# Optimization experiments

Hardware: AMD Instinct MI355X
Metric: run time of the kernel (lower is better)

Reference implementation:

```python
import jax, jax.numpy as jnp
import numpy as np

E, H, D = 512, 8, 64          # embed_dim, num_heads, head_dim
MAX_SUM = 128                  # max_summary (embedding table has MAX_SUM+1 rows, row 0 = padding)
SCALE = D ** -0.5


def _linear(x, w, b):
    y = jnp.einsum('...i,oi->...o', x, w)
    return y if b is None else y + b


def setup_inputs() -> dict:
    key = jax.random.key(0)
    ks = jax.random.split(key, 16)
    R, B, S = 2048, 2, 128

    def xav(k, shape, gain=1.0):
        fan_in, fan_out = shape[1], shape[0]
        a = gain * np.sqrt(6.0 / (fan_in + fan_out))
        return jax.random.uniform(k, shape, jnp.float32, -a, a)

    g = 1.0 / np.sqrt(2.0)
    embed_table = jax.random.normal(ks[0], (MAX_SUM + 1, E), jnp.float32) * 0.02
    embed_table = embed_table.at[0].set(0.0)  # padding_idx=0
    return {
        'reg_x': jax.random.normal(ks[1], (R, B, E), jnp.float32),
        'sum_token_ids': jax.random.randint(ks[2], (B, S), 0, MAX_SUM),
        'sum_len': S,
        'reg_len': R,
        'embed_table': embed_table,
        'wq1': xav(ks[3], (E, E), g), 'bq1': jnp.zeros((E,), jnp.float32),
        'wq2': xav(ks[4], (E, E), g), 'bq2': jnp.zeros((E,), jnp.float32),
        'wk': xav(ks[5], (E, E), g),  'bk': jnp.zeros((E,), jnp.float32),
        'wv': xav(ks[6], (E, E), g),  'bv': jnp.zeros((E,), jnp.float32),
        'wo': xav(ks[7], (E, E)),     'bo': jnp.zeros((E,), jnp.float32),
        'sum_gate_w': xav(ks[8], (E, E)),
        'reg_gate_w': xav(ks[9], (E, E)),
        'gate_bias': jax.random.normal(ks[10], (E,), jnp.float32),
    }


def reference(reg_x, sum_token_ids, sum_len, reg_len, embed_table,
              wq1, bq1, wq2, bq2, wk, bk, wv, bv, wo, bo,
              sum_gate_w, reg_gate_w, gate_bias):
    R, B, _ = reg_x.shape
    S = sum_token_ids.shape[1]

    # regular keys/values (shared across all stages)
    reg_k = _linear(reg_x, wk, bk).reshape(R, B, H, D)
    reg_v = _linear(reg_x, wv, bv).reshape(R, B, H, D)

    # ---- stage 1: summary queries (learned summary embeddings) attend to regular tokens
    sum_q = embed_table[sum_token_ids.T].reshape(S, B, H, D)  # [S,B,H,D]
    scores_sr = jnp.einsum('sbhd,rbhd->bhsr', sum_q * SCALE, reg_k)
    w_sr = jax.nn.softmax(scores_sr, axis=-1)
    sum_x2 = jnp.einsum('bhsr,rbhd->sbhd', w_sr, reg_v)       # summary K=V for stage 2

    # ---- stage 2: regular queries attend to summary tokens
    reg_q1 = _linear(reg_x, wq1, bq1).reshape(R, B, H, D)
    scores_rs = jnp.einsum('rbhd,sbhd->bhrs', reg_q1 * SCALE, sum_x2)
    w_rs = jax.nn.softmax(scores_rs, axis=-1)
    sum_output = jnp.einsum('bhrs,sbhd->rbhd', w_rs, sum_x2).reshape(R, B, E)

    # ---- stage 3: regular self-attention
    reg_q2 = _linear(reg_x, wq2, bq2).reshape(R, B, H, D)
    scores_rr = jnp.einsum('qbhd,kbhd->bhqk', reg_q2 * SCALE, reg_k)
    w_rr = jax.nn.softmax(scores_rr, axis=-1)
    reg_output = jnp.einsum('bhqk,kbhd->qbhd', w_rr, reg_v).reshape(R, B, E)

    # ---- gated fusion of summary path and regular path
    gate = jax.nn.sigmoid(_linear(sum_output, sum_gate_w, None)
                          + _linear(reg_output, reg_gate_w, None) + gate_bias)
    attn_output = gate * sum_output + (1.0 - gate) * reg_output
    return _linear(attn_output, wo, bo)
```

## Files before the change

kernel.cpp:

```cpp
#include <hip/hip_runtime.h>
#include <cstdint>
#include <cstddef>

constexpr int R_ = 2048;
constexpr int B_ = 2;
constexpr int S_ = 128;
constexpr int E_ = 512;
constexpr int H_ = 8;
constexpr int D_ = 64;
constexpr int N_ = R_ * B_;
constexpr float SCALE_ = 0.125f;
constexpr float LOG2E_ = 1.44269504088896340736f;
constexpr float SLOG2E_ = SCALE_ * LOG2E_;

typedef short bf8_t __attribute__((ext_vector_type(8)));
typedef float f32x4 __attribute__((ext_vector_type(4)));
typedef float f32x16 __attribute__((ext_vector_type(16)));
typedef unsigned u32x4 __attribute__((ext_vector_type(4)));

#define MFMA16(a, b, c) __builtin_amdgcn_mfma_f32_16x16x32_bf16((a), (b), (c), 0, 0, 0)
#define MFMA32(a, b, c) __builtin_amdgcn_mfma_f32_32x32x16_bf16((a), (b), (c), 0, 0, 0)

__device__ __forceinline__ unsigned short f2bf(float f) {
  unsigned u = __builtin_bit_cast(unsigned, f);
  unsigned r = u + 0x7FFFu + ((u >> 16) & 1u);
  return (unsigned short)(r >> 16);
}
__device__ __forceinline__ float bf2f(unsigned short h) {
  unsigned u = ((unsigned)h) << 16;
  return __builtin_bit_cast(float, u);
}
__device__ __forceinline__ int kvperm(int kv) {
  return (kv & ~15) | (kv & 3) | ((kv & 4) << 1) | ((kv & 8) >> 1);
}

struct WSplitJob { const float* src; unsigned short* dst; };
struct WSplit7 { WSplitJob j[7]; };

__global__ __launch_bounds__(256)
void fused_split_kernel(const float* __restrict__ reg_x, unsigned short* __restrict__ Apair,
                        WSplit7 P, const float* __restrict__ table,
                        const int* __restrict__ ids,
                        unsigned short* __restrict__ sqhi, unsigned short* __restrict__ sqlo)
{
  const int bx = blockIdx.x;
  const int tid = threadIdx.x;
  if (bx < 8192) {
    const int idx = bx * 256 + tid;
    const int r = idx >> 9, c = idx & 511;
    const float v = reg_x[idx];
    const unsigned short hi = f2bf(v);
    unsigned short* d = Apair + ((size_t)r << 10) + c;
    d[0] = hi; d[512] = f2bf(v - bf2f(hi));
  } else if (bx < 15360) {
    const int bj = bx - 8192;
    const WSplitJob jb = P.j[bj >> 10];
    const int idx = (bj & 1023) * 256 + tid;
    const int r = idx >> 9, c = idx & 511;
    const float v = jb.src[idx];
    const unsigned short hi = f2bf(v);
    const unsigned short lo = f2bf(v - bf2f(hi));
    unsigned short* d = jb.dst + (size_t)r * 1536 + c;
    d[0] = hi; d[512] = hi; d[1024] = lo;
  } else {
    const int idx = (bx - 15360) * 256 + tid;
    const int d = idx & 63;
    const int s = (idx >> 6) & 127;
    const int h = (idx >> 13) & 7;
    const int b = idx >> 16;
    const float v = table[(size_t)ids[b * S_ + s] * E_ + h * 64 + d] * SLOG2E_;
    const unsigned short hi = f2bf(v);
    sqhi[idx] = hi;
    sqlo[idx] = f2bf(v - bf2f(hi));
  }
}

struct GemmOut {
  const unsigned short* W;
  const float* bias;
  float scale;
  float* Cf;
  unsigned short* hi;
  unsigned short* lo;
  int mode;
};
struct GemmOuts4 { GemmOut o[4]; };

__global__ __launch_bounds__(256, 4)
void gemm_split_kernel(const unsigned short* __restrict__ A, GemmOuts4 P)
{
  const GemmOut g = P.o[blockIdx.z];
  __shared__ unsigned short As[128][48];
  __shared__ unsigned short Ws[64][48];

  const int tid = threadIdx.x;
  const int w = tid >> 6;
  const int l = tid & 63;
  const int lr = l & 15;
  const int lg = l >> 4;
  const int n0 = blockIdx.x * 128;
  const int o0 = blockIdx.y * 64;

  f32x4 acc[2][4];
#pragma unroll
  for (int m = 0; m < 2; ++m)
#pragma unroll
    for (int n = 0; n < 4; ++n) acc[m][n] = (f32x4){0.f, 0.f, 0.f, 0.f};

  const int ar = tid >> 1;
  const int ac = (tid & 1) * 16;
  const int wr = tid >> 2;
  const int wc = (tid & 3) * 8;

  bf8_t ra0 = *(const bf8_t*)(A + (size_t)(n0 + ar) * 1024 + ac);
  bf8_t ra1 = *(const bf8_t*)(A + (size_t)(n0 + ar) * 1024 + ac + 8);
  bf8_t rw0 = *(const bf8_t*)(g.W + (size_t)(o0 + wr) * 1536 + wc);

  for (int k0 = 0; k0 < 1536; k0 += 32) {
    __syncthreads();
    *(bf8_t*)&As[ar][ac] = ra0;
    *(bf8_t*)&As[ar][ac + 8] = ra1;
    *(bf8_t*)&Ws[wr][wc] = rw0;
    __syncthreads();
    if (k0 + 32 < 1536) {
      const int ak = (k0 + 32) & 1023;
      ra0 = *(const bf8_t*)(A + (size_t)(n0 + ar) * 1024 + ak + ac);
      ra1 = *(const bf8_t*)(A + (size_t)(n0 + ar) * 1024 + ak + ac + 8);
      rw0 = *(const bf8_t*)(g.W + (size_t)(o0 + wr) * 1536 + k0 + 32 + wc);
    }

    bf8_t bvs[4];
#pragma unroll
    for (int n = 0; n < 4; ++n)
      bvs[n] = *(const bf8_t*)&Ws[n * 16 + lr][lg * 8];
#pragma unroll
    for (int m = 0; m < 2; ++m) {
      bf8_t av = *(const bf8_t*)&As[w * 32 + m * 16 + lr][lg * 8];
#pragma unroll
      for (int n = 0; n < 4; ++n)
        acc[m][n] = MFMA16(av, bvs[n], acc[m][n]);
    }
  }

#pragma unroll
  for (int m = 0; m < 2; ++m)
#pragma unroll
    for (int n = 0; n < 4; ++n)
#pragma unroll
      for (int r = 0; r < 4; ++r) {
        const int row = n0 + w * 32 + m * 16 + lg * 4 + r;
        const int col = o0 + n * 16 + lr;
        float v = acc[m][n][r];
        if (g.bias) v += g.bias[col];
        v *= g.scale;
        if (g.mode == 0) {
          g.Cf[((size_t)row << 9) + col] = v;
        } else {
          const int bb = row & 1, rr = row >> 1;
          const int hh = col >> 6, dd = col & 63;
          size_t id;
          if (g.mode == 1) id = (((size_t)(bb * H_ + hh) * R_) + rr) * 64 + dd;
          else             id = (((size_t)(bb * H_ + hh) * 64) + dd) * R_ + kvperm(rr);
          const unsigned short hv = f2bf(v);
          g.hi[id] = hv;
          g.lo[id] = f2bf(v - bf2f(hv));
        }
      }
}

__global__ __launch_bounds__(256, 4)
void gate_blend_gemm_kernel(const unsigned short* __restrict__ A1,
                            const unsigned short* __restrict__ A2,
                            const unsigned short* __restrict__ W1,
                            const unsigned short* __restrict__ W2,
                            const float* __restrict__ gb,
                            unsigned short* __restrict__ attnP)
{
  __shared__ unsigned short As[128][48];
  __shared__ unsigned short Ws[64][48];

  const int tid = threadIdx.x;
  const int w = tid >> 6;
  const int l = tid & 63;
  const int lr = l & 15;
  const int lg = l >> 4;
  const int n0 = blockIdx.x * 128;
  const int o0 = blockIdx.y * 64;

  f32x4 acc[2][4];
#pragma unroll
  for (int m = 0; m < 2; ++m)
#pragma unroll
    for (int n = 0; n < 4; ++n) acc[m][n] = (f32x4){0.f, 0.f, 0.f, 0.f};

  const int ar = tid >> 1;
  const int ac = (tid & 1) * 16;
  const int wr = tid >> 2;
  const int wc = (tid & 3) * 8;

  auto aP = [&](int kk) {
    const unsigned short* Ax = (kk < 48) ? A1 : A2;
    const int k0 = ((kk < 48) ? kk : kk - 48) * 32;
    return Ax + (size_t)(n0 + ar) * 1024 + (k0 & 1023) + ac;
  };
  auto wP = [&](int kk) {
    const unsigned short* Wx = (kk < 48) ? W1 : W2;
    const int k0 = ((kk < 48) ? kk : kk - 48) * 32;
    return Wx + (size_t)(o0 + wr) * 1536 + k0 + wc;
  };

  bf8_t ra0 = *(const bf8_t*)aP(0);
  bf8_t ra1 = *(const bf8_t*)(aP(0) + 8);
  bf8_t rw0 = *(const bf8_t*)wP(0);

  for (int kk = 0; kk < 96; ++kk) {
    __syncthreads();
    *(bf8_t*)&As[ar][ac] = ra0;
    *(bf8_t*)&As[ar][ac + 8] = ra1;
    *(bf8_t*)&Ws[wr][wc] = rw0;
    __syncthreads();
    if (kk + 1 < 96) {
      ra0 = *(const bf8_t*)aP(kk + 1);
      ra1 = *(const bf8_t*)(aP(kk + 1) + 8);
      rw0 = *(const bf8_t*)wP(kk + 1);
    }

    bf8_t bvs[4];
#pragma unroll
    for (int n = 0; n < 4; ++n)
      bvs[n] = *(const bf8_t*)&Ws[n * 16 + lr][lg * 8];
#pragma unroll
    for (int m = 0; m < 2; ++m) {
      bf8_t av = *(const bf8_t*)&As[w * 32 + m * 16 + lr][lg * 8];
#pragma unroll
      for (int n = 0; n < 4; ++n)
        acc[m][n] = MFMA16(av, bvs[n], acc[m][n]);
    }
  }

#pragma unroll
  for (int m = 0; m < 2; ++m)
#pragma unroll
    for (int n = 0; n < 4; ++n)
#pragma unroll
      for (int r = 0; r < 4; ++r) {
        const int row = n0 + w * 32 + m * 16 + lg * 4 + r;
        const int col = o0 + n * 16 + lr;
        const float t = acc[m][n][r] + gb[col];
        const float gt = 1.0f / (1.0f + __expf(-t));
        const size_t base = (size_t)row << 10;
        const float so = bf2f(A1[base + col]) + bf2f(A1[base + 512 + col]);
        const float ro = bf2f(A2[base + col]) + bf2f(A2[base + 512 + col]);
        const float a = gt * so + (1.0f - gt) * ro;
        const unsigned short hv = f2bf(a);
        attnP[base + col] = hv;
        attnP[base + 512 + col] = f2bf(a - bf2f(hv));
      }
}

__global__ __launch_bounds__(256, 2)
void flash_partial_kernel(const unsigned short* __restrict__ Qhi, const unsigned short* __restrict__ Qlo,
                          const unsigned short* __restrict__ Khi, const unsigned short* __restrict__ Klo,
                          const unsigned short* __restrict__ VtHi, const unsigned short* __restrict__ VtLo,
                          int q_len, int kv_len, int chunk, int zsplit, int out_mode,
                          float* __restrict__ accA, float* __restrict__ accB,
                          float* __restrict__ mlP, unsigned short* __restrict__ OutP)
{
  __shared__ unsigned short KsH[64][72];
  __shared__ unsigned short KsL[64][72];
  __shared__ unsigned short VsH[64][72];
  __shared__ unsigned short VsL[64][72];

  const int tid = threadIdx.x;
  const int w = tid >> 6;
  const int l = tid & 63;
  const int lq = l & 31;
  const int hi = l >> 5;
  const int bh = blockIdx.y;
  const int q0 = blockIdx.x * 128;
  const int c = blockIdx.z;
  const int kvbeg = c * chunk;
  const int kvend = kvbeg + chunk;
  const int qrow = q0 + w * 32 + lq;

  bf8_t qh[4], ql[4];
  {
    const size_t qbase = ((size_t)bh * q_len + qrow) * 64;
#pragma unroll
    for (int kd = 0; kd < 4; ++kd) {
      qh[kd] = *(const bf8_t*)(Qhi + qbase + kd * 16 + hi * 8);
      ql[kd] = *(const bf8_t*)(Qlo + qbase + kd * 16 + hi * 8);
    }
  }

  f32x16 acc0 = {0,0,0,0,0,0,0,0,0,0,0,0,0,0,0,0};
  f32x16 acc1 = {0,0,0,0,0,0,0,0,0,0,0,0,0,0,0,0};
  float mrow = -INFINITY;
  float lrow = 0.0f;

  const int sr = tid >> 2;
  const int sc = (tid & 3) * 16;

  bf8_t rkh[2], rkl[2], rvh[2], rvl[2];
  {
    const size_t kb = ((size_t)bh * kv_len + kvbeg + sr) * 64 + sc;
    rkh[0] = *(const bf8_t*)(Khi + kb);  rkh[1] = *(const bf8_t*)(Khi + kb + 8);
    rkl[0] = *(const bf8_t*)(Klo + kb);  rkl[1] = *(const bf8_t*)(Klo + kb + 8);
    const size_t vb = ((size_t)bh * 64 + sr) * kv_len + kvbeg + sc;
    rvh[0] = *(const bf8_t*)(VtHi + vb); rvh[1] = *(const bf8_t*)(VtHi + vb + 8);
    rvl[0] = *(const bf8_t*)(VtLo + vb); rvl[1] = *(const bf8_t*)(VtLo + vb + 8);
  }

  for (int kv0 = kvbeg; kv0 < kvend; kv0 += 64) {
    __syncthreads();
    *(bf8_t*)&KsH[sr][sc] = rkh[0];  *(bf8_t*)&KsH[sr][sc + 8] = rkh[1];
    *(bf8_t*)&KsL[sr][sc] = rkl[0];  *(bf8_t*)&KsL[sr][sc + 8] = rkl[1];
    *(bf8_t*)&VsH[sr][sc] = rvh[0];  *(bf8_t*)&VsH[sr][sc + 8] = rvh[1];
    *(bf8_t*)&VsL[sr][sc] = rvl[0];  *(bf8_t*)&VsL[sr][sc + 8] = rvl[1];
    __syncthreads();
    if (kv0 + 64 < kvend) {
      const size_t kb = ((size_t)bh * kv_len + kv0 + 64 + sr) * 64 + sc;
      rkh[0] = *(const bf8_t*)(Khi + kb);  rkh[1] = *(const bf8_t*)(Khi + kb + 8);
      rkl[0] = *(const bf8_t*)(Klo + kb);  rkl[1] = *(const bf8_t*)(Klo + kb + 8);
      const size_t vb = ((size_t)bh * 64 + sr) * kv_len + kv0 + 64 + sc;
      rvh[0] = *(const bf8_t*)(VtHi + vb); rvh[1] = *(const bf8_t*)(VtHi + vb + 8);
      rvl[0] = *(const bf8_t*)(VtLo + vb); rvl[1] = *(const bf8_t*)(VtLo + vb + 8);
    }

    f32x16 s0 = {0,0,0,0,0,0,0,0,0,0,0,0,0,0,0,0};
    f32x16 s1 = {0,0,0,0,0,0,0,0,0,0,0,0,0,0,0,0};
    __builtin_amdgcn_s_setprio(1);
#pragma unroll
    for (int kd = 0; kd < 4; ++kd) {
      const bf8_t kfh0 = *(const bf8_t*)&KsH[lq][kd * 16 + hi * 8];
      const bf8_t kfl0 = *(const bf8_t*)&KsL[lq][kd * 16 + hi * 8];
      s0 = MFMA32(kfh0, qh[kd], s0);
      s0 = MFMA32(kfh0, ql[kd], s0);
      s0 = MFMA32(kfl0, qh[kd], s0);
      const bf8_t kfh1 = *(const bf8_t*)&KsH[32 + lq][kd * 16 + hi * 8];
      const bf8_t kfl1 = *(const bf8_t*)&KsL[32 + lq][kd * 16 + hi * 8];
      s1 = MFMA32(kfh1, qh[kd], s1);
      s1 = MFMA32(kfh1, ql[kd], s1);
      s1 = MFMA32(kfl1, qh[kd], s1);
    }
    __builtin_amdgcn_s_setprio(0);

    float mx = fmaxf(s0[0], s1[0]);
#pragma unroll
    for (int r = 1; r < 16; ++r) mx = fmaxf(mx, fmaxf(s0[r], s1[r]));
    mx = fmaxf(mx, __shfl_xor(mx, 32));
    if (mx > mrow + 8.0f) {
      const float f = exp2f(mrow - mx);
      mrow = mx;
      lrow *= f;
#pragma unroll
      for (int r = 0; r < 16; ++r) { acc0[r] *= f; acc1[r] *= f; }
    }
    float ts = 0.f;
#pragma unroll
    for (int r = 0; r < 16; ++r) { s0[r] = exp2f(s0[r] - mrow); ts += s0[r]; }
#pragma unroll
    for (int r = 0; r < 16; ++r) { s1[r] = exp2f(s1[r] - mrow); ts += s1[r]; }
    ts += __shfl_xor(ts, 32);
    lrow += ts;

    bf8_t pah[4], pal[4];
#pragma unroll
    for (int n = 0; n < 2; ++n)
#pragma unroll
      for (int ks = 0; ks < 2; ++ks) {
        u32x4 hp, lp;
#pragma unroll
        for (int p2 = 0; p2 < 4; ++p2) {
          const float a = n ? s1[ks * 8 + p2 * 2]     : s0[ks * 8 + p2 * 2];
          const float b = n ? s1[ks * 8 + p2 * 2 + 1] : s0[ks * 8 + p2 * 2 + 1];
          const unsigned ua = __builtin_bit_cast(unsigned, a);
          const unsigned ub = __builtin_bit_cast(unsigned, b);
          hp[p2] = (ua >> 16) | (ub & 0xFFFF0000u);
          const float la = a - __builtin_bit_cast(float, ua & 0xFFFF0000u);
          const float lb = b - __builtin_bit_cast(float, ub & 0xFFFF0000u);
          lp[p2] = (__builtin_bit_cast(unsigned, la) >> 16) |
                   (__builtin_bit_cast(unsigned, lb) & 0xFFFF0000u);
        }
        pah[n * 2 + ks] = __builtin_bit_cast(bf8_t, hp);
        pal[n * 2 + ks] = __builtin_bit_cast(bf8_t, lp);
      }

    __builtin_amdgcn_s_setprio(1);
#pragma unroll
    for (int n = 0; n < 2; ++n)
#pragma unroll
      for (int ks = 0; ks < 2; ++ks) {
        const int vcol = n * 32 + ks * 16 + hi * 8;
        const bf8_t ph = pah[n * 2 + ks];
        const bf8_t pl = pal[n * 2 + ks];
        {
          const bf8_t vfh = *(const bf8_t*)&VsH[lq][vcol];
          const bf8_t vfl = *(const bf8_t*)&VsL[lq][vcol];
          acc0 = MFMA32(vfh, ph, acc0);
          acc0 = MFMA32(vfh, pl, acc0);
          acc0 = MFMA32(vfl, ph, acc0);
        }
        {
          const bf8_t vfh = *(const bf8_t*)&VsH[32 + lq][vcol];
          const bf8_t vfl = *(const bf8_t*)&VsL[32 + lq][vcol];
          acc1 = MFMA32(vfh, ph, acc1);
          acc1 = MFMA32(vfh, pl, acc1);
          acc1 = MFMA32(vfl, ph, acc1);
        }
      }
    __builtin_amdgcn_s_setprio(0);
  }

  if (out_mode == 0) {
    const size_t cstride = (size_t)16 * q_len * 64;
    float* accbase = (c < zsplit) ? accA + (size_t)c * cstride
                                  : accB + (size_t)(c - zsplit) * cstride;
    float* rowp = accbase + ((size_t)bh * q_len + qrow) * 64;
#pragma unroll
    for (int rg = 0; rg < 4; ++rg) {
      *(float4*)(rowp + rg * 8 + hi * 4) =
          make_float4(acc0[rg * 4 + 0], acc0[rg * 4 + 1], acc0[rg * 4 + 2], acc0[rg * 4 + 3]);
      *(float4*)(rowp + 32 + rg * 8 + hi * 4) =
          make_float4(acc1[rg * 4 + 0], acc1[rg * 4 + 1], acc1[rg * 4 + 2], acc1[rg * 4 + 3]);
    }
    if (l < 32) {
      const int q = q0 + w * 32 + l;
      *(float2*)&mlP[((size_t)(c * 16 + bh) * q_len + q) * 2] = make_float2(mrow, lrow);
    }
  } else {
    const float inv = 1.0f / lrow;
    const int b = bh >> 3, h = bh & 7;
    const size_t base = ((size_t)qrow * B_ + b) << 10;
#pragma unroll
    for (int hd = 0; hd < 2; ++hd)
#pragma unroll
      for (int rg = 0; rg < 4; ++rg) {
        const int col = h * 64 + hd * 32 + rg * 8 + hi * 4;
        ushort4 hv4, lv4;
#pragma unroll
        for (int i = 0; i < 4; ++i) {
          const float v = (hd ? acc1[rg * 4 + i] : acc0[rg * 4 + i]) * inv;
          const unsigned short hv = f2bf(v);
          ((unsigned short*)&hv4)[i] = hv;
          ((unsigned short*)&lv4)[i] = f2bf(v - bf2f(hv));
        }
        *(ushort4*)&OutP[base + col] = hv4;
        *(ushort4*)&OutP[base + 512 + col] = lv4;
      }
  }
}

__global__ __launch_bounds__(256)
void merge_x2_kernel(const float* __restrict__ acc, const float* __restrict__ ml,
                     unsigned short* __restrict__ X2hi, unsigned short* __restrict__ X2lo,
                     unsigned short* __restrict__ X2Thi, unsigned short* __restrict__ X2Tlo)
{
  const int idx = blockIdx.x * 256 + threadIdx.x;
  const int d = idx & 63;
  const int q = (idx >> 6) & 127;
  const int bh = idx >> 13;
  float M = -INFINITY;
#pragma unroll
  for (int c = 0; c < 16; ++c)
    M = fmaxf(M, ml[((size_t)(c * 16 + bh) * 128 + q) * 2]);
  float ls = 0.f, o = 0.f;
#pragma unroll
  for (int c = 0; c < 16; ++c) {
    const size_t mi = ((size_t)(c * 16 + bh) * 128 + q) * 2;
    const float wgt = exp2f(ml[mi] - M);
    ls += wgt * ml[mi + 1];
    o += wgt * acc[(size_t)c * 131072 + ((size_t)bh * 128 + q) * 64 + d];
  }
  const float v = o / ls;
  const unsigned short hv = f2bf(v);
  const unsigned short lv = f2bf(v - bf2f(hv));
  X2hi[((size_t)bh * 128 + q) * 64 + d] = hv;
  X2lo[((size_t)bh * 128 + q) * 64 + d] = lv;
  const int qp = kvperm(q);
  X2Thi[((size_t)bh * 64 + d) * 128 + qp] = hv;
  X2Tlo[((size_t)bh * 64 + d) * 128 + qp] = lv;
}

__global__ __launch_bounds__(256)
void merge_rows_kernel(const float* __restrict__ accA, const float* __restrict__ accB,
                       const float* __restrict__ ml, unsigned short* __restrict__ OutP)
{
  const int idx = blockIdx.x * 256 + threadIdx.x;
  const int d = idx & 63;
  const int q = (idx >> 6) & 2047;
  const int bh = idx >> 17;
  const size_t mi0 = ((size_t)bh * 2048 + q) * 2;
  const size_t mi1 = ((size_t)(16 + bh) * 2048 + q) * 2;
  const float m0 = ml[mi0], m1 = ml[mi1];
  const float M = fmaxf(m0, m1);
  const float w0 = exp2f(m0 - M), w1 = exp2f(m1 - M);
  const float ls = w0 * ml[mi0 + 1] + w1 * ml[mi1 + 1];
  const size_t aoff = ((size_t)bh * 2048 + q) * 64 + d;
  const float v = (w0 * accA[aoff] + w1 * accB[aoff]) / ls;
  const int b = bh >> 3, h = bh & 7;
  const size_t nrow = (size_t)q * B_ + b;
  const int col = h * 64 + d;
  const unsigned short hv = f2bf(v);
  OutP[nrow * 1024 + col] = hv;
  OutP[nrow * 1024 + 512 + col] = f2bf(v - bf2f(hv));
}

extern "C" void kernel_launch(void* const* d_in, const int* in_sizes, int n_in,
                              void* d_out, int out_size, void* d_ws, size_t ws_size,
                              hipStream_t stream)
{
  const float* reg_x = (const float*)d_in[0];
  const int*   ids   = (const int*)d_in[1];
  const float* table = (const float*)d_in[4];
  const float* wq1 = (const float*)d_in[5];  const float* bq1 = (const float*)d_in[6];
  const float* wq2 = (const float*)d_in[7];  const float* bq2 = (const float*)d_in[8];
  const float* wk  = (const float*)d_in[9];  const float* bk  = (const float*)d_in[10];
  const float* wv  = (const float*)d_in[11]; const float* bv  = (const float*)d_in[12];
  const float* wo  = (const float*)d_in[13]; const float* bo  = (const float*)d_in[14];
  const float* sgw = (const float*)d_in[15];
  const float* rgw = (const float*)d_in[16];
  const float* gb  = (const float*)d_in[17];
  float* out = (float*)d_out;
  char* W = (char*)d_ws;

  const size_t WSLOT  = 1572864;
  const size_t oApair = 0;
  const size_t oW     = 8388608;
  const size_t oKhi   = oW + 7 * WSLOT;
  const size_t oKlo   = oKhi + 4194304;
  const size_t oVtHi  = oKlo + 4194304;
  const size_t oVtLo  = oVtHi + 4194304;
  const size_t oQ1hi  = oVtLo + 4194304;
  const size_t oQ1lo  = oQ1hi + 4194304;
  const size_t oQ2hi  = oQ1lo + 4194304;
  const size_t oQ2lo  = oQ2hi + 4194304;
  const size_t oAcc1  = oQ2lo + 4194304;
  const size_t oSQhi  = oAcc1 + 8388608;
  const size_t oSQlo  = oSQhi + 262144;
  const size_t oX2hi  = oSQlo + 262144;
  const size_t oX2lo  = oX2hi + 262144;
  const size_t oX2Thi = oX2lo + 262144;
  const size_t oX2Tlo = oX2Thi + 262144;
  const size_t oMl    = oX2Tlo + 262144;

  auto U16 = [&](size_t off) { return (unsigned short*)(W + off); };
  auto F32 = [&](size_t off) { return (float*)(W + off); };
  unsigned short* Apair  = U16(oApair);
  unsigned short* Wk3    = U16(oW + 0 * WSLOT);
  unsigned short* Wv3    = U16(oW + 1 * WSLOT);
  unsigned short* Wq13   = U16(oW + 2 * WSLOT);
  unsigned short* Wq23   = U16(oW + 3 * WSLOT);
  unsigned short* Wsg3   = U16(oW + 4 * WSLOT);
  unsigned short* Wrg3   = U16(oW + 5 * WSLOT);
  unsigned short* Wo3    = U16(oW + 6 * WSLOT);
  float*          accS   = F32(oApair);
  float*          accB3  = F32(oAcc1);
  float*          mlP    = F32(oMl);
  unsigned short* sout_p = U16(oQ1hi);
  unsigned short* rout_p = U16(oQ2hi);
  unsigned short* attn_p = U16(oKhi);

  const dim3 blk(256);

  WSplit7 ws7;
  ws7.j[0] = WSplitJob{wk,  Wk3};
  ws7.j[1] = WSplitJob{wv,  Wv3};
  ws7.j[2] = WSplitJob{wq1, Wq13};
  ws7.j[3] = WSplitJob{wq2, Wq23};
  ws7.j[4] = WSplitJob{sgw, Wsg3};
  ws7.j[5] = WSplitJob{rgw, Wrg3};
  ws7.j[6] = WSplitJob{wo,  Wo3};
  fused_split_kernel<<<15872, blk, 0, stream>>>(reg_x, Apair, ws7, table, ids,
                                                U16(oSQhi), U16(oSQlo));

  GemmOuts4 proj;
  proj.o[0].W = Wk3;  proj.o[0].bias = bk;  proj.o[0].scale = 1.0f;    proj.o[0].Cf = nullptr;
  proj.o[0].hi = U16(oKhi);  proj.o[0].lo = U16(oKlo);  proj.o[0].mode = 1;
  proj.o[1].W = Wv3;  proj.o[1].bias = bv;  proj.o[1].scale = 1.0f;    proj.o[1].Cf = nullptr;
  proj.o[1].hi = U16(oVtHi); proj.o[1].lo = U16(oVtLo); proj.o[1].mode = 2;
  proj.o[2].W = Wq13; proj.o[2].bias = bq1; proj.o[2].scale = SLOG2E_; proj.o[2].Cf = nullptr;
  proj.o[2].hi = U16(oQ1hi); proj.o[2].lo = U16(oQ1lo); proj.o[2].mode = 1;
  proj.o[3].W = Wq23; proj.o[3].bias = bq2; proj.o[3].scale = SLOG2E_; proj.o[3].Cf = nullptr;
  proj.o[3].hi = U16(oQ2hi); proj.o[3].lo = U16(oQ2lo); proj.o[3].mode = 1;
  gemm_split_kernel<<<dim3(32, 8, 4), blk, 0, stream>>>(Apair, proj);

  flash_partial_kernel<<<dim3(1, 16, 16), blk, 0, stream>>>(
      U16(oSQhi), U16(oSQlo), U16(oKhi), U16(oKlo), U16(oVtHi), U16(oVtLo),
      S_, R_, 128, 16, 0, accS, accS, mlP, nullptr);
  merge_x2_kernel<<<512, blk, 0, stream>>>(accS, mlP,
      U16(oX2hi), U16(oX2lo), U16(oX2Thi), U16(oX2Tlo));

  flash_partial_kernel<<<dim3(16, 16, 1), blk, 0, stream>>>(
      U16(oQ1hi), U16(oQ1lo), U16(oX2hi), U16(oX2lo), U16(oX2Thi), U16(oX2Tlo),
      R_, S_, 128, 1, 1, accS, accS, mlP, sout_p);

  flash_partial_kernel<<<dim3(16, 16, 2), blk, 0, stream>>>(
      U16(oQ2hi), U16(oQ2lo), U16(oKhi), U16(oKlo), U16(oVtHi), U16(oVtLo),
      R_, R_, 1024, 1, 0, accS, accB3, mlP, nullptr);
  merge_rows_kernel<<<8192, blk, 0, stream>>>(accS, accB3, mlP, rout_p);

  gate_blend_gemm_kernel<<<dim3(32, 8), blk, 0, stream>>>(
      sout_p, rout_p, Wsg3, Wrg3, gb, attn_p);

  GemmOuts4 gf;
  gf.o[0].W = Wo3; gf.o[0].bias = bo; gf.o[0].scale = 1.0f; gf.o[0].Cf = out;
  gf.o[0].hi = nullptr; gf.o[0].lo = nullptr; gf.o[0].mode = 0;
  gf.o[1] = gf.o[0]; gf.o[2] = gf.o[0]; gf.o[3] = gf.o[0];
  gemm_split_kernel<<<dim3(32, 8, 1), blk, 0, stream>>>(attn_p, gf);
}
```

Measured before the change: 230.5 us.

## Rewrite GEMMs with 128x128 tiles, direct-to-LDS loads, and rebalance self-attention split

Replaces the 128x64 register-staged GEMM with a 128x128-tile kernel that uses global_load_lds double buffering and raised MFMA priority. The gate GEMM becomes two batched plain GEMMs followed by a separate elementwise blend kernel. The stage-3 self-attention KV split goes from two halves to an uneven three-way split (1024/512/512) with a three-way merge. The workspace layout is reshuffled and packing uses v_perm. The aim is more data reuse per tile, fewer LDS round trips, and better occupancy, at the cost of extra fp32 traffic for the blend and an extra merge input.

```diff
diff --git a/kernel.cpp b/kernel.cpp
--- a/kernel.cpp
+++ b/kernel.cpp
@@ -32,6 +32,11 @@
 }
 __device__ __forceinline__ int kvperm(int kv) {
   return (kv & ~15) | (kv & 3) | ((kv & 4) << 1) | ((kv & 8) >> 1);
+}
+__device__ __forceinline__ void gload16(const unsigned short* g, unsigned short* l) {
+  __builtin_amdgcn_global_load_lds(
+      (const __attribute__((address_space(1))) unsigned*)g,
+      (__attribute__((address_space(3))) unsigned*)l, 16, 0, 0);
 }
 
 struct WSplitJob { const float* src; unsigned short* dst; };
@@ -75,7 +80,8 @@
   }
 }
 
-struct GemmOut {
+struct GOut {
+  const unsigned short* A;
   const unsigned short* W;
   const float* bias;
   float scale;
@@ -84,72 +90,82 @@
   unsigned short* lo;
   int mode;
 };
-struct GemmOuts4 { GemmOut o[4]; };
-
-__global__ __launch_bounds__(256, 4)
-void gemm_split_kernel(const unsigned short* __restrict__ A, GemmOuts4 P)
-{
-  const GemmOut g = P.o[blockIdx.z];
-  __shared__ unsigned short As[128][48];
-  __shared__ unsigned short Ws[64][48];
+struct GOuts4 { GOut o[4]; };
+
+__global__ __launch_bounds__(256, 2)
+void gemm128_kernel(GOuts4 P)
+{
+  const GOut g = P.o[blockIdx.z];
+  __shared__ unsigned short As[2][4096];
+  __shared__ unsigned short Ws[2][4096];
 
   const int tid = threadIdx.x;
   const int w = tid >> 6;
   const int l = tid & 63;
   const int lr = l & 15;
   const int lg = l >> 4;
+  const int wr = (w >> 1) * 64;
+  const int wc = (w & 1) * 64;
   const int n0 = blockIdx.x * 128;
-  const int o0 = blockIdx.y * 64;
-
-  f32x4 acc[2][4];
-#pragma unroll
-  for (int m = 0; m < 2; ++m)
+  const int o0 = blockIdx.y * 128;
+
+  const int srow = w * 32 + (l >> 2);
+  const int scol = (l & 3) * 8;
+  const unsigned short* A0 = g.A + (size_t)(n0 + srow) * 1024 + scol;
+  const unsigned short* A1 = A0 + (size_t)16 * 1024;
+  const unsigned short* W0 = g.W + (size_t)(o0 + srow) * 1536 + scol;
+  const unsigned short* W1 = W0 + (size_t)16 * 1536;
+
+  f32x4 acc[4][4];
+#pragma unroll
+  for (int m = 0; m < 4; ++m)
 #pragma unroll
     for (int n = 0; n < 4; ++n) acc[m][n] = (f32x4){0.f, 0.f, 0.f, 0.f};
 
-  const int ar = tid >> 1;
-  const int ac = (tid & 1) * 16;
-  const int wr = tid >> 2;
-  const int wc = (tid & 3) * 8;
-
-  bf8_t ra0 = *(const bf8_t*)(A + (size_t)(n0 + ar) * 1024 + ac);
-  bf8_t ra1 = *(const bf8_t*)(A + (size_t)(n0 + ar) * 1024 + ac + 8);
-  bf8_t rw0 = *(const bf8_t*)(g.W + (size_t)(o0 + wr) * 1536 + wc);
-
-  for (int k0 = 0; k0 < 1536; k0 += 32) {
+  {
+    gload16(A0, &As[0][w * 1024]);
+    gload16(A1, &As[0][w * 1024 + 512]);
+    gload16(W0, &Ws[0][w * 1024]);
+    gload16(W1, &Ws[0][w * 1024 + 512]);
+  }
+  __syncthreads();
+
+  int buf = 0;
+  for (int t = 0; t < 48; ++t) {
+    if (t + 1 < 48) {
+      const int ak = ((t + 1) * 32) & 1023;
+      const int wk = (t + 1) * 32;
+      gload16(A0 + ak, &As[buf ^ 1][w * 1024]);
+      gload16(A1 + ak, &As[buf ^ 1][w * 1024 + 512]);
+      gload16(W0 + wk, &Ws[buf ^ 1][w * 1024]);
+      gload16(W1 + wk, &Ws[buf ^ 1][w * 1024 + 512]);
+    }
+    bf8_t av[4], bv[4];
+#pragma unroll
+    for (int m = 0; m < 4; ++m)
+      av[m] = *(const bf8_t*)&As[buf][(wr + m * 16 + lr) * 32 + lg * 8];
+#pragma unroll
+    for (int n = 0; n < 4; ++n)
+      bv[n] = *(const bf8_t*)&Ws[buf][(wc + n * 16 + lr) * 32 + lg * 8];
+    __builtin_amdgcn_s_setprio(1);
+#pragma unroll
+    for (int m = 0; m < 4; ++m)
+#pragma unroll
+      for (int n = 0; n < 4; ++n)
+        acc[m][n] = MFMA16(av[m], bv[n], acc[m][n]);
+    __builtin_amdgcn_s_setprio(0);
     __syncthreads();
-    *(bf8_t*)&As[ar][ac] = ra0;
-    *(bf8_t*)&As[ar][ac + 8] = ra1;
-    *(bf8_t*)&Ws[wr][wc] = rw0;
-    __syncthreads();
-    if (k0 + 32 < 1536) {
-      const int ak = (k0 + 32) & 1023;
-      ra0 = *(const bf8_t*)(A + (size_t)(n0 + ar) * 1024 + ak + ac);
-      ra1 = *(const bf8_t*)(A + (size_t)(n0 + ar) * 1024 + ak + ac + 8);
-      rw0 = *(const bf8_t*)(g.W + (size_t)(o0 + wr) * 1536 + k0 + 32 + wc);
-    }
-
-    bf8_t bvs[4];
+    buf ^= 1;
+  }
+
+#pragma unroll
+  for (int m = 0; m < 4; ++m)
 #pragma unroll
     for (int n = 0; n < 4; ++n)
-      bvs[n] = *(const bf8_t*)&Ws[n * 16 + lr][lg * 8];
-#pragma unroll
-    for (int m = 0; m < 2; ++m) {
-      bf8_t av = *(const bf8_t*)&As[w * 32 + m * 16 + lr][lg * 8];
-#pragma unroll
-      for (int n = 0; n < 4; ++n)
-        acc[m][n] = MFMA16(av, bvs[n], acc[m][n]);
-    }
-  }
-
-#pragma unroll
-  for (int m = 0; m < 2; ++m)
-#pragma unroll
-    for (int n = 0; n < 4; ++n)
 #pragma unroll
       for (int r = 0; r < 4; ++r) {
-        const int row = n0 + w * 32 + m * 16 + lg * 4 + r;
-        const int col = o0 + n * 16 + lr;
+        const int row = n0 + wr + m * 16 + lg * 4 + r;
+        const int col = o0 + wc + n * 16 + lr;
         float v = acc[m][n][r];
         if (g.bias) v += g.bias[col];
         v *= g.scale;
@@ -168,102 +184,31 @@
       }
 }
 
-__global__ __launch_bounds__(256, 4)
-void gate_blend_gemm_kernel(const unsigned short* __restrict__ A1,
-                            const unsigned short* __restrict__ A2,
-                            const unsigned short* __restrict__ W1,
-                            const unsigned short* __restrict__ W2,
-                            const float* __restrict__ gb,
-                            unsigned short* __restrict__ attnP)
-{
-  __shared__ unsigned short As[128][48];
-  __shared__ unsigned short Ws[64][48];
-
-  const int tid = threadIdx.x;
-  const int w = tid >> 6;
-  const int l = tid & 63;
-  const int lr = l & 15;
-  const int lg = l >> 4;
-  const int n0 = blockIdx.x * 128;
-  const int o0 = blockIdx.y * 64;
-
-  f32x4 acc[2][4];
-#pragma unroll
-  for (int m = 0; m < 2; ++m)
-#pragma unroll
-    for (int n = 0; n < 4; ++n) acc[m][n] = (f32x4){0.f, 0.f, 0.f, 0.f};
-
-  const int ar = tid >> 1;
-  const int ac = (tid & 1) * 16;
-  const int wr = tid >> 2;
-  const int wc = (tid & 3) * 8;
-
-  auto aP = [&](int kk) {
-    const unsigned short* Ax = (kk < 48) ? A1 : A2;
-    const int k0 = ((kk < 48) ? kk : kk - 48) * 32;
-    return Ax + (size_t)(n0 + ar) * 1024 + (k0 & 1023) + ac;
-  };
-  auto wP = [&](int kk) {
-    const unsigned short* Wx = (kk < 48) ? W1 : W2;
-    const int k0 = ((kk < 48) ? kk : kk - 48) * 32;
-    return Wx + (size_t)(o0 + wr) * 1536 + k0 + wc;
-  };
-
-  bf8_t ra0 = *(const bf8_t*)aP(0);
-  bf8_t ra1 = *(const bf8_t*)(aP(0) + 8);
-  bf8_t rw0 = *(const bf8_t*)wP(0);
-
-  for (int kk = 0; kk < 96; ++kk) {
-    __syncthreads();
-    *(bf8_t*)&As[ar][ac] = ra0;
-    *(bf8_t*)&As[ar][ac + 8] = ra1;
-    *(bf8_t*)&Ws[wr][wc] = rw0;
-    __syncthreads();
-    if (kk + 1 < 96) {
-      ra0 = *(const bf8_t*)aP(kk + 1);
-      ra1 = *(const bf8_t*)(aP(kk + 1) + 8);
-      rw0 = *(const bf8_t*)wP(kk + 1);
-    }
-
-    bf8_t bvs[4];
-#pragma unroll
-    for (int n = 0; n < 4; ++n)
-      bvs[n] = *(const bf8_t*)&Ws[n * 16 + lr][lg * 8];
-#pragma unroll
-    for (int m = 0; m < 2; ++m) {
-      bf8_t av = *(const bf8_t*)&As[w * 32 + m * 16 + lr][lg * 8];
-#pragma unroll
-      for (int n = 0; n < 4; ++n)
-        acc[m][n] = MFMA16(av, bvs[n], acc[m][n]);
-    }
-  }
-
-#pragma unroll
-  for (int m = 0; m < 2; ++m)
-#pragma unroll
-    for (int n = 0; n < 4; ++n)
-#pragma unroll
-      for (int r = 0; r < 4; ++r) {
-        const int row = n0 + w * 32 + m * 16 + lg * 4 + r;
-        const int col = o0 + n * 16 + lr;
-        const float t = acc[m][n][r] + gb[col];
-        const float gt = 1.0f / (1.0f + __expf(-t));
-        const size_t base = (size_t)row << 10;
-        const float so = bf2f(A1[base + col]) + bf2f(A1[base + 512 + col]);
-        const float ro = bf2f(A2[base + col]) + bf2f(A2[base + 512 + col]);
-        const float a = gt * so + (1.0f - gt) * ro;
-        const unsigned short hv = f2bf(a);
-        attnP[base + col] = hv;
-        attnP[base + 512 + col] = f2bf(a - bf2f(hv));
-      }
+__global__ __launch_bounds__(256)
+void blend_kernel(const float* __restrict__ t1, const float* __restrict__ t2,
+                  const float* __restrict__ gb,
+                  const unsigned short* __restrict__ sp, const unsigned short* __restrict__ rp,
+                  unsigned short* __restrict__ ap)
+{
+  const int idx = blockIdx.x * 256 + threadIdx.x;
+  const int e = idx & 511;
+  const size_t base = (size_t)(idx >> 9) << 10;
+  const float so = bf2f(sp[base + e]) + bf2f(sp[base + 512 + e]);
+  const float ro = bf2f(rp[base + e]) + bf2f(rp[base + 512 + e]);
+  const float x = t1[idx] + t2[idx] + gb[e];
+  const float gt = 1.0f / (1.0f + __expf(-x));
+  const float a = gt * so + (1.0f - gt) * ro;
+  const unsigned short hv = f2bf(a);
+  ap[base + e] = hv;
+  ap[base + 512 + e] = f2bf(a - bf2f(hv));
 }
 
 __global__ __launch_bounds__(256, 2)
 void flash_partial_kernel(const unsigned short* __restrict__ Qhi, const unsigned short* __restrict__ Qlo,
                           const unsigned short* __restrict__ Khi, const unsigned short* __restrict__ Klo,
                           const unsigned short* __restrict__ VtHi, const unsigned short* __restrict__ VtLo,
-                          int q_len, int kv_len, int chunk, int zsplit, int out_mode,
-                          float* __restrict__ accA, float* __restrict__ accB,
+                          int q_len, int kv_len, int firstlen, int chunk, int zsplit, int out_mode,
+                          float* __restrict__ acc0p, float* __restrict__ acc1p, float* __restrict__ acc2p,
                           float* __restrict__ mlP, unsigned short* __restrict__ OutP)
 {
   __shared__ unsigned short KsH[64][72];
@@ -279,8 +224,8 @@
   const int bh = blockIdx.y;
   const int q0 = blockIdx.x * 128;
   const int c = blockIdx.z;
-  const int kvbeg = c * chunk;
-  const int kvend = kvbeg + chunk;
+  const int kvbeg = (c == 0) ? 0 : firstlen + (c - 1) * chunk;
+  const int kvend = kvbeg + ((c == 0) ? firstlen : chunk);
   const int qrow = q0 + w * 32 + lq;
 
   bf8_t qh[4], ql[4];
@@ -365,6 +310,7 @@
     lrow += ts;
 
     bf8_t pah[4], pal[4];
+    const unsigned sel = 0x07060302u;
 #pragma unroll
     for (int n = 0; n < 2; ++n)
 #pragma unroll
@@ -376,11 +322,11 @@
           const float b = n ? s1[ks * 8 + p2 * 2 + 1] : s0[ks * 8 + p2 * 2 + 1];
           const unsigned ua = __builtin_bit_cast(unsigned, a);
           const unsigned ub = __builtin_bit_cast(unsigned, b);
-          hp[p2] = (ua >> 16) | (ub & 0xFFFF0000u);
+          hp[p2] = __builtin_amdgcn_perm(ub, ua, sel);
           const float la = a - __builtin_bit_cast(float, ua & 0xFFFF0000u);
           const float lb = b - __builtin_bit_cast(float, ub & 0xFFFF0000u);
-          lp[p2] = (__builtin_bit_cast(unsigned, la) >> 16) |
-                   (__builtin_bit_cast(unsigned, lb) & 0xFFFF0000u);
+          lp[p2] = __builtin_amdgcn_perm(__builtin_bit_cast(unsigned, lb),
+                                         __builtin_bit_cast(unsigned, la), sel);
         }
         pah[n * 2 + ks] = __builtin_bit_cast(bf8_t, hp);
         pal[n * 2 + ks] = __builtin_bit_cast(bf8_t, lp);
@@ -414,8 +360,9 @@
 
   if (out_mode == 0) {
     const size_t cstride = (size_t)16 * q_len * 64;
-    float* accbase = (c < zsplit) ? accA + (size_t)c * cstride
-                                  : accB + (size_t)(c - zsplit) * cstride;
+    float* accbase;
+    if (zsplit == 16) accbase = acc0p + (size_t)c * cstride;
+    else accbase = (c == 0) ? acc0p : (c == 1) ? acc1p : acc2p;
     float* rowp = accbase + ((size_t)bh * q_len + qrow) * 64;
 #pragma unroll
     for (int rg = 0; rg < 4; ++rg) {
@@ -483,21 +430,23 @@
 }
 
 __global__ __launch_bounds__(256)
-void merge_rows_kernel(const float* __restrict__ accA, const float* __restrict__ accB,
-                       const float* __restrict__ ml, unsigned short* __restrict__ OutP)
+void merge_rows3_kernel(const float* __restrict__ a0, const float* __restrict__ a1,
+                        const float* __restrict__ a2, const float* __restrict__ ml,
+                        unsigned short* __restrict__ OutP)
 {
   const int idx = blockIdx.x * 256 + threadIdx.x;
   const int d = idx & 63;
   const int q = (idx >> 6) & 2047;
   const int bh = idx >> 17;
-  const size_t mi0 = ((size_t)bh * 2048 + q) * 2;
-  const size_t mi1 = ((size_t)(16 + bh) * 2048 + q) * 2;
-  const float m0 = ml[mi0], m1 = ml[mi1];
-  const float M = fmaxf(m0, m1);
-  const float w0 = exp2f(m0 - M), w1 = exp2f(m1 - M);
-  const float ls = w0 * ml[mi0 + 1] + w1 * ml[mi1 + 1];
-  const size_t aoff = ((size_t)bh * 2048 + q) * 64 + d;
-  const float v = (w0 * accA[aoff] + w1 * accB[aoff]) / ls;
+  const size_t mb = (size_t)bh * 2048 + q;
+  const float m0 = ml[mb * 2],                 l0 = ml[mb * 2 + 1];
+  const float m1 = ml[(mb + 16 * 2048) * 2],   l1 = ml[(mb + 16 * 2048) * 2 + 1];
+  const float m2 = ml[(mb + 32 * 2048) * 2],   l2 = ml[(mb + 32 * 2048) * 2 + 1];
+  const float M = fmaxf(m0, fmaxf(m1, m2));
+  const float w0 = exp2f(m0 - M), w1 = exp2f(m1 - M), w2 = exp2f(m2 - M);
+  const float ls = w0 * l0 + w1 * l1 + w2 * l2;
+  const size_t aoff = mb * 64 + d;
+  const float v = (w0 * a0[aoff] + w1 * a1[aoff] + w2 * a2[aoff]) / ls;
   const int b = bh >> 3, h = bh & 7;
   const size_t nrow = (size_t)q * B_ + b;
   const int col = h * 64 + d;
@@ -527,8 +476,15 @@
   const size_t WSLOT  = 1572864;
   const size_t oApair = 0;
   const size_t oW     = 8388608;
-  const size_t oKhi   = oW + 7 * WSLOT;
-  const size_t oKlo   = oKhi + 4194304;
+  const size_t oSQhi  = oW + 7 * WSLOT;
+  const size_t oSQlo  = oSQhi + 262144;
+  const size_t oX2hi  = oSQlo + 262144;
+  const size_t oX2lo  = oX2hi + 262144;
+  const size_t oX2Thi = oX2lo + 262144;
+  const size_t oX2Tlo = oX2Thi + 262144;
+  const size_t oAcc2  = oW + 3 * WSLOT;
+  const size_t oK     = oAcc2 + 8388608;
+  const size_t oKlo   = oK + 4194304;
   const size_t oVtHi  = oKlo + 4194304;
   const size_t oVtLo  = oVtHi + 4194304;
   const size_t oQ1hi  = oVtLo + 4194304;
@@ -536,30 +492,27 @@
   const size_t oQ2hi  = oQ1lo + 4194304;
   const size_t oQ2lo  = oQ2hi + 4194304;
   const size_t oAcc1  = oQ2lo + 4194304;
-  const size_t oSQhi  = oAcc1 + 8388608;
-  const size_t oSQlo  = oSQhi + 262144;
-  const size_t oX2hi  = oSQlo + 262144;
-  const size_t oX2lo  = oX2hi + 262144;
-  const size_t oX2Thi = oX2lo + 262144;
-  const size_t oX2Tlo = oX2Thi + 262144;
-  const size_t oMl    = oX2Tlo + 262144;
+  const size_t oMl    = oAcc1 + 8388608;
 
   auto U16 = [&](size_t off) { return (unsigned short*)(W + off); };
   auto F32 = [&](size_t off) { return (float*)(W + off); };
-  unsigned short* Apair  = U16(oApair);
-  unsigned short* Wk3    = U16(oW + 0 * WSLOT);
-  unsigned short* Wv3    = U16(oW + 1 * WSLOT);
-  unsigned short* Wq13   = U16(oW + 2 * WSLOT);
-  unsigned short* Wq23   = U16(oW + 3 * WSLOT);
-  unsigned short* Wsg3   = U16(oW + 4 * WSLOT);
-  unsigned short* Wrg3   = U16(oW + 5 * WSLOT);
-  unsigned short* Wo3    = U16(oW + 6 * WSLOT);
-  float*          accS   = F32(oApair);
-  float*          accB3  = F32(oAcc1);
-  float*          mlP    = F32(oMl);
+  unsigned short* Apair = U16(oApair);
+  unsigned short* Wo3   = U16(oW + 0 * WSLOT);
+  unsigned short* Wsg3  = U16(oW + 1 * WSLOT);
+  unsigned short* Wrg3  = U16(oW + 2 * WSLOT);
+  unsigned short* Wk3   = U16(oW + 3 * WSLOT);
+  unsigned short* Wv3   = U16(oW + 4 * WSLOT);
+  unsigned short* Wq13  = U16(oW + 5 * WSLOT);
+  unsigned short* Wq23  = U16(oW + 6 * WSLOT);
+  float*          accS  = F32(oApair);
+  float*          acc1  = F32(oAcc1);
+  float*          acc2  = F32(oAcc2);
+  float*          mlP   = F32(oMl);
   unsigned short* sout_p = U16(oQ1hi);
   unsigned short* rout_p = U16(oQ2hi);
-  unsigned short* attn_p = U16(oKhi);
+  unsigned short* attn_p = U16(oK);
+  float*          t1    = F32(oApair);
+  float*          t2    = F32(oAcc1);
 
   const dim3 blk(256);
 
@@ -574,38 +527,38 @@
   fused_split_kernel<<<15872, blk, 0, stream>>>(reg_x, Apair, ws7, table, ids,
                                                 U16(oSQhi), U16(oSQlo));
 
-  GemmOuts4 proj;
-  proj.o[0].W = Wk3;  proj.o[0].bias = bk;  proj.o[0].scale = 1.0f;    proj.o[0].Cf = nullptr;
-  proj.o[0].hi = U16(oKhi);  proj.o[0].lo = U16(oKlo);  proj.o[0].mode = 1;
-  proj.o[1].W = Wv3;  proj.o[1].bias = bv;  proj.o[1].scale = 1.0f;    proj.o[1].Cf = nullptr;
-  proj.o[1].hi = U16(oVtHi); proj.o[1].lo = U16(oVtLo); proj.o[1].mode = 2;
-  proj.o[2].W = Wq13; proj.o[2].bias = bq1; proj.o[2].scale = SLOG2E_; proj.o[2].Cf = nullptr;
-  proj.o[2].hi = U16(oQ1hi); proj.o[2].lo = U16(oQ1lo); proj.o[2].mode = 1;
-  proj.o[3].W = Wq23; proj.o[3].bias = bq2; proj.o[3].scale = SLOG2E_; proj.o[3].Cf = nullptr;
-  proj.o[3].hi = U16(oQ2hi); proj.o[3].lo = U16(oQ2lo); proj.o[3].mode = 1;
-  gemm_split_kernel<<<dim3(32, 8, 4), blk, 0, stream>>>(Apair, proj);
+  GOuts4 proj;
+  proj.o[0] = GOut{Apair, Wk3,  bk,  1.0f,    nullptr, U16(oK),    U16(oKlo),  1};
+  proj.o[1] = GOut{Apair, Wv3,  bv,  1.0f,    nullptr, U16(oVtHi), U16(oVtLo), 2};
+  proj.o[2] = GOut{Apair, Wq13, bq1, SLOG2E_, nullptr, U16(oQ1hi), U16(oQ1lo), 1};
+  proj.o[3] = GOut{Apair, Wq23, bq2, SLOG2E_, nullptr, U16(oQ2hi), U16(oQ2lo), 1};
+  gemm128_kernel<<<dim3(32, 4, 4), blk, 0, stream>>>(proj);
 
   flash_partial_kernel<<<dim3(1, 16, 16), blk, 0, stream>>>(
-      U16(oSQhi), U16(oSQlo), U16(oKhi), U16(oKlo), U16(oVtHi), U16(oVtLo),
-      S_, R_, 128, 16, 0, accS, accS, mlP, nullptr);
+      U16(oSQhi), U16(oSQlo), U16(oK), U16(oKlo), U16(oVtHi), U16(oVtLo),
+      S_, R_, 128, 128, 16, 0, accS, nullptr, nullptr, mlP, nullptr);
   merge_x2_kernel<<<512, blk, 0, stream>>>(accS, mlP,
       U16(oX2hi), U16(oX2lo), U16(oX2Thi), U16(oX2Tlo));
 
   flash_partial_kernel<<<dim3(16, 16, 1), blk, 0, stream>>>(
       U16(oQ1hi), U16(oQ1lo), U16(oX2hi), U16(oX2lo), U16(oX2Thi), U16(oX2Tlo),
-      R_, S_, 128, 1, 1, accS, accS, mlP, sout_p);
-
-  flash_partial_kernel<<<dim3(16, 16, 2), blk, 0, stream>>>(
-      U16(oQ2hi), U16(oQ2lo), U16(oKhi), U16(oKlo), U16(oVtHi), U16(oVtLo),
-      R_, R_, 1024, 1, 0, accS, accB3, mlP, nullptr);
-  merge_rows_kernel<<<8192, blk, 0, stream>>>(accS, accB3, mlP, rout_p);
-
-  gate_blend_gemm_kernel<<<dim3(32, 8), blk, 0, stream>>>(
-      sout_p, rout_p, Wsg3, Wrg3, gb, attn_p);
-
-  GemmOuts4 gf;
-  gf.o[0].W = Wo3; gf.o[0].bias = bo; gf.o[0].scale = 1.0f; gf.o[0].Cf = out;
-  gf.o[0].hi = nullptr; gf.o[0].lo = nullptr; gf.o[0].mode = 0;
+      R_, S_, 128, 128, 1, 1, accS, nullptr, nullptr, mlP, sout_p);
+
+  flash_partial_kernel<<<dim3(16, 16, 3), blk, 0, stream>>>(
+      U16(oQ2hi), U16(oQ2lo), U16(oK), U16(oKlo), U16(oVtHi), U16(oVtLo),
+      R_, R_, 1024, 512, 3, 0, accS, acc1, acc2, mlP, nullptr);
+  merge_rows3_kernel<<<8192, blk, 0, stream>>>(accS, acc1, acc2, mlP, rout_p);
+
+  GOuts4 gate;
+  gate.o[0] = GOut{sout_p, Wsg3, nullptr, 1.0f, t1, nullptr, nullptr, 0};
+  gate.o[1] = GOut{rout_p, Wrg3, nullptr, 1.0f, t2, nullptr, nullptr, 0};
+  gate.o[2] = gate.o[0]; gate.o[3] = gate.o[0];
+  gemm128_kernel<<<dim3(32, 4, 2), blk, 0, stream>>>(gate);
+
+  blend_kernel<<<8192, blk, 0, stream>>>(t1, t2, gb, sout_p, rout_p, attn_p);
+
+  GOuts4 gf;
+  gf.o[0] = GOut{attn_p, Wo3, bo, 1.0f, out, nullptr, nullptr, 0};
   gf.o[1] = gf.o[0]; gf.o[2] = gf.o[0]; gf.o[3] = gf.o[0];
-  gemm_split_kernel<<<dim3(32, 8, 1), blk, 0, stream>>>(attn_p, gf);
-}
+  gemm128_kernel<<<dim3(32, 4, 1), blk, 0, stream>>>(gf);
+}
```

New measurement: 240.3 us. +4.2%, slower.
